# Optimization experiments

Hardware: AMD Instinct MI355X
Metric: run time of the kernel (lower is better)

Reference implementation:

```python
import jax, jax.numpy as jnp
import numpy as np

EPS = 1e-14
RHO = 8.0


def _normalize(x):
    return x / jnp.linalg.norm(x, axis=-1, keepdims=True)


def setup_inputs() -> dict:
    key = jax.random.key(0)
    ks = jax.random.split(key, 12)
    B, D = 4096, 1024
    f = lambda k: _normalize(jax.random.normal(k, (B, D), dtype=jnp.float32))
    pos = lambda k: jax.random.uniform(k, (B, 1), dtype=jnp.float32, minval=0.1, maxval=1.0)
    return {
        "im_feat": f(ks[0]),
        "tt_feat": f(ks[1]),
        "rim_feat": f(ks[2]),
        "rtt_feat": f(ks[3]),
        "remote_u_im": pos(ks[4]),
        "remote_u_tt": pos(ks[5]),
        "loss1_im": pos(ks[6]),
        "loss1_tt": pos(ks[7]),
        "u_im": pos(ks[8]),
        "u_tt": pos(ks[9]),
        "logit_scale": 10.0 * jnp.ones((1,), dtype=jnp.float32),
        "offset": 0,
    }


def _pairwise_loss(rim, rtt, im, tt, logit_scale, offset):
    # features1 = remote, features2 = local (as in forward(): pairwise_loss(remote_features, features, ...))
    sim_image = rim @ tt.T                                  # [B1, B2]
    sim_text = rtt @ im.T                                   # [B1, B2]
    diag_sim = jnp.sum(rim * rtt, axis=-1, keepdims=True)   # [B1, 1]
    exp_im = jnp.exp((sim_image - diag_sim) * logit_scale)
    exp_tt = jnp.exp((sim_text - diag_sim) * logit_scale)
    B1, B2 = sim_image.shape
    # mask zeros the shifted diagonal: equivalent to subtracting the diagonal entry from the row sum
    cols = (jnp.arange(B1) + offset)[:, None]               # [B1, 1]
    rw_sum = B2 - 1 if B1 <= B2 else B2 * (B1 - 1) / B1
    loss_im = (jnp.sum(exp_im, axis=-1, keepdims=True)
               - jnp.take_along_axis(exp_im, cols, axis=1)) / rw_sum
    loss_tt = (jnp.sum(exp_tt, axis=-1, keepdims=True)
               - jnp.take_along_axis(exp_tt, cols, axis=1)) / rw_sum
    return loss_im, loss_tt


def reference(im_feat, tt_feat, rim_feat, rtt_feat, remote_u_im, remote_u_tt,
              loss1_im, loss1_tt, u_im, u_tt, logit_scale, offset):
    loss2_im, loss2_tt = _pairwise_loss(rim_feat, rtt_feat, im_feat, tt_feat, logit_scale, offset)
    pg1 = loss1_im / (u_im + EPS) + loss1_tt / (u_tt + EPS)
    pg2 = loss2_im / (remote_u_im + EPS) + loss2_tt / (remote_u_tt + EPS)
    loss = (jnp.mean(pg1) + jnp.mean(pg2)) / 2
    # multiply_tau branch
    ls = logit_scale[0]
    loss = loss / jax.lax.stop_gradient(ls)
    loss = loss + RHO / ls
    loss = loss + jnp.mean(jnp.log(u_im) + jnp.log(u_tt)) / 2 / ls
    return loss
```

## Files before the change

### kernel.cpp

```cpp
#include <hip/hip_runtime.h>
#include <hip/hip_bf16.h>

#define EPSF 1e-14f
#define RHOF 8.0f

typedef __attribute__((ext_vector_type(4))) float f32x4;
typedef __attribute__((ext_vector_type(8))) int   i32x8;
typedef __attribute__((ext_vector_type(2))) unsigned long long u64x2;

#define AS_GLOBAL __attribute__((address_space(1)))
#define AS_LDS    __attribute__((address_space(3)))


__global__ __launch_bounds__(256) void prep_fp8(
    const float* __restrict__ im,  const float* __restrict__ tt,
    const float* __restrict__ rim, const float* __restrict__ rtt,
    unsigned char* __restrict__ bIm,  unsigned char* __restrict__ bTt,
    unsigned char* __restrict__ bRim, unsigned char* __restrict__ bRtt,
    float* __restrict__ S_im, float* __restrict__ S_tt,
    float* __restrict__ diag, float* __restrict__ red,
    int D, int spm )
{
    __shared__ unsigned char L[8 * 1024];
    const int b = blockIdx.x;
    const int tid = threadIdx.x;
    const int nConv = 4 * spm;
    if (b < nConv) {
        int mIdx = b / spm;
        int slab = b - mIdx * spm;
        const float* src = (mIdx == 0) ? rim : (mIdx == 1) ? tt
                          : (mIdx == 2) ? rtt : im;
        unsigned char* dst = (mIdx == 0) ? bRim : (mIdx == 1) ? bTt
                            : (mIdx == 2) ? bRtt : bIm;
        const float* srow = src + (size_t)slab * 8 * D;
        const int n4 = (8 * D) >> 2;
        for (int idx = tid; idx < n4; idx += 256) {
            float4 v = *(const float4*)(srow + idx * 4);
            int pk = __builtin_amdgcn_cvt_pk_fp8_f32(v.x, v.y, 0, false);
            pk     = __builtin_amdgcn_cvt_pk_fp8_f32(v.z, v.w, pk, true);
            *(int*)&L[idx * 4] = pk;
        }
        __syncthreads();
        const int kTiles = D >> 7;
        const int rb = (slab * 8) >> 7;
        const int r0loc = (slab * 8) & 127;
        for (int g = tid; g < (D >> 1); g += 256) {
            int kb  = g >> 6;
            int rem = g & 63;
            int rl  = rem >> 3;
            int p   = rem & 7;
            int r   = slab * 8 + rl;
            int c   = p ^ (r & 7);
            const unsigned char* lb = &L[rl * D + kb * 128 + c * 16];
            u64x2 o = *(const u64x2*)lb;
            char* outp = (char*)dst
                       + ((size_t)(rb * kTiles + kb) * 1024
                          + (size_t)(r0loc + rl) * 8 + p) * 16;
            *(u64x2*)outp = o;
        }
    } else {
        int db = b - nConv;
        if (db == 0 && tid < 8) red[tid] = 0.f;
        if (tid < 4) { S_im[db * 4 + tid] = 0.f; S_tt[db * 4 + tid] = 0.f; }
        int row  = db * 4 + (tid >> 6);
        int lane = tid & 63;
        const float* a = rim + (size_t)row * D;
        const float* c = rtt + (size_t)row * D;
        float s = 0.f;
        for (int k = lane * 4; k < D; k += 256) {
            float4 av = *(const float4*)(a + k);
            float4 cv = *(const float4*)(c + k);
            s += av.x * cv.x + av.y * cv.y + av.z * cv.z + av.w * cv.w;
        }
        #pragma unroll
        for (int m2 = 1; m2 < 64; m2 <<= 1) s += __shfl_xor(s, m2, 64);
        if (lane == 0) diag[row] = s;
    }
}

__global__ __launch_bounds__(512, 2) void gemm_expsum(
    const unsigned char* __restrict__ A0, const unsigned char* __restrict__ B0,
    float* __restrict__ S0,
    const unsigned char* __restrict__ A1, const unsigned char* __restrict__ B1,
    float* __restrict__ S1,
    const float* __restrict__ logit_scale, const int* __restrict__ offset,
    int Bn, int D)
{
    const int z = blockIdx.z;
    const unsigned char* A = z ? A1 : A0;
    const unsigned char* B = z ? B1 : B0;
    float* S = z ? S1 : S0;

    __shared__ unsigned char As[2][32768];
    __shared__ unsigned char Bs[2][32768];

    const int tid  = threadIdx.x;
    const int wave = tid >> 6;
    const int lane = tid & 63;
    const int lo   = lane & 15;
    const int qd   = lane >> 4;
    const int wm   = wave >> 2;
    const int wn   = wave & 3;
    const int offA = ((2 * qd) ^ (lo & 7)) * 16;

    const int nx  = gridDim.x;
    const int nwg = nx * gridDim.y;
    int wg = blockIdx.y * nx + blockIdx.x;
    int swz = ((nwg & 7) == 0) ? ((wg & 7) * (nwg >> 3) + (wg >> 3)) : wg;
    const int by = swz / nx;
    const int bx = swz - by * nx;

    const int kTiles = D >> 7;
    const unsigned char* Atile = A + (size_t)(2 * by) * kTiles * 16384;
    const unsigned char* Btile = B + (size_t)(2 * bx) * kTiles * 16384;

    const int half = wave >> 1;
    const int part = wave & 1;
    const unsigned char* ownerG =
        (half < 2) ? Atile + (size_t)half * kTiles * 16384
                   : Btile + (size_t)(half - 2) * kTiles * 16384;
    const unsigned char* ownerGL = ownerG + part * 8192 + lane * 16;
    const int ownerLoff = (half & 1) * 16384 + part * 8192;
    const bool ownerIsA = (half < 2);

    auto stageOwner = [&](int buf, int kb) {
        const unsigned char* g = ownerGL + (size_t)kb * 16384;
        unsigned char* l = (ownerIsA ? &As[buf][0] : &Bs[buf][0]) + ownerLoff;
        #pragma unroll
        for (int q = 0; q < 8; ++q)
            __builtin_amdgcn_global_load_lds(
                (const AS_GLOBAL unsigned int*)(g + q * 1024),
                (AS_LDS unsigned int*)(l + q * 1024), 16, 0, 0);
    };

    f32x4 acc[8][4];
    #pragma unroll
    for (int i = 0; i < 8; ++i)
        #pragma unroll
        for (int j = 0; j < 4; ++j)
            acc[i][j] = (f32x4){0.f, 0.f, 0.f, 0.f};

    const int aOff0 = wm * 16384 + lo * 128 + offA;
    const int bOff0 = (wn >> 1) * 16384 + ((wn & 1) * 64 + lo) * 128 + offA;

    stageOwner(0, 0);
    asm volatile("s_waitcnt vmcnt(0)" ::: "memory");
    __builtin_amdgcn_s_barrier();

    for (int kb = 0; kb < kTiles; ++kb) {
        const int cur = kb & 1;
        if (kb + 1 < kTiles)
            stageOwner(1 - cur, kb + 1);

        i32x8 bq[4];
        #pragma unroll
        for (int tj = 0; tj < 4; ++tj) {
            const int ba = bOff0 + tj * 2048;
            union { int4 h[2]; i32x8 v; } u;
            u.h[0] = *(const int4*)&Bs[cur][ba];
            u.h[1] = *(const int4*)&Bs[cur][ba ^ 16];
            bq[tj] = u.v;
        }

        #pragma unroll
        for (int ph = 0; ph < 4; ++ph) {
            const int ti0 = 2 * ph;
            union { int4 h[2]; i32x8 v; } ua0, ua1;
            {
                const int aa0 = aOff0 + ti0 * 2048;
                ua0.h[0] = *(const int4*)&As[cur][aa0];
                ua0.h[1] = *(const int4*)&As[cur][aa0 ^ 16];
                const int aa1 = aOff0 + (ti0 + 1) * 2048;
                ua1.h[0] = *(const int4*)&As[cur][aa1];
                ua1.h[1] = *(const int4*)&As[cur][aa1 ^ 16];
            }
            __builtin_amdgcn_s_barrier();
            __builtin_amdgcn_s_setprio(1);
            #pragma unroll
            for (int tj = 0; tj < 4; ++tj)
                acc[ti0][tj] = __builtin_amdgcn_mfma_scale_f32_16x16x128_f8f6f4(
                    ua0.v, bq[tj], acc[ti0][tj],
                    0, 0, 0, 127, 0, 127);
            #pragma unroll
            for (int tj = 0; tj < 4; ++tj)
                acc[ti0 + 1][tj] = __builtin_amdgcn_mfma_scale_f32_16x16x128_f8f6f4(
                    ua1.v, bq[tj], acc[ti0 + 1][tj],
                    0, 0, 0, 127, 0, 127);
            __builtin_amdgcn_s_setprio(0);
            __builtin_amdgcn_s_barrier();
        }

        if (kb + 1 < kTiles) {
            asm volatile("s_waitcnt vmcnt(0)" ::: "memory");
            __builtin_amdgcn_s_barrier();
        }
    }

    const float ls = logit_scale[0];
    const int offs = offset[0];
    const int rowBase = by * 256 + wm * 128;
    const int colBase = bx * 256 + wn * 64;
    #pragma unroll
    for (int ti = 0; ti < 8; ++ti) {
        #pragma unroll
        for (int r = 0; r < 4; ++r) {
            int gi = rowBase + 16 * ti + 4 * qd + r;
            float rs = 0.f;
            #pragma unroll
            for (int tj = 0; tj < 4; ++tj) {
                int gj = colBase + 16 * tj + lo;
                float e = __expf(ls * acc[ti][tj][r]);
                if (gj == gi + offs) e = 0.f;
                rs += e;
            }
            #pragma unroll
            for (int m = 1; m < 16; m <<= 1) rs += __shfl_xor(rs, m, 64);
            if (lo == 0) atomicAdd(&S[gi], rs);
        }
    }
}

__global__ __launch_bounds__(256) void final_kernel(
    const float* __restrict__ S_im, const float* __restrict__ S_tt,
    const float* __restrict__ diag,
    const float* __restrict__ ru_im, const float* __restrict__ ru_tt,
    const float* __restrict__ l1_im, const float* __restrict__ l1_tt,
    const float* __restrict__ u_im,  const float* __restrict__ u_tt,
    const float* __restrict__ logit_scale, float* __restrict__ red,
    float* __restrict__ out, int Bn)
{
    const float ls = logit_scale[0];
    const float inv_rw = 1.0f / (float)(Bn - 1);
    const int gid = blockIdx.x * 256 + threadIdx.x;
    float pg = 0.f, lg = 0.f;
    for (int i = gid; i < Bn; i += 8 * 256) {
        float p1 = l1_im[i] / (u_im[i] + EPSF) + l1_tt[i] / (u_tt[i] + EPSF);
        float dd = expf(-ls * diag[i]);
        float p2 = dd * S_im[i] * inv_rw / (ru_im[i] + EPSF)
                 + dd * S_tt[i] * inv_rw / (ru_tt[i] + EPSF);
        pg += p1 + p2;
        lg += logf(u_im[i]) + logf(u_tt[i]);
    }
    __shared__ float sp[256], sl[256];
    sp[threadIdx.x] = pg; sl[threadIdx.x] = lg;
    __syncthreads();
    for (int s = 128; s > 0; s >>= 1) {
        if (threadIdx.x < s) { sp[threadIdx.x] += sp[threadIdx.x + s];
                               sl[threadIdx.x] += sl[threadIdx.x + s]; }
        __syncthreads();
    }
    if (threadIdx.x == 0) {
        atomicAdd(&red[0], sp[0]);
        atomicAdd(&red[1], sl[0]);
        __threadfence();
        int t = atomicAdd((int*)&red[2], 1);
        if (t == gridDim.x - 1) {
            float pgSum = atomicAdd(&red[0], 0.f);
            float lgSum = atomicAdd(&red[1], 0.f);
            float loss = ((pgSum / (float)Bn) * 0.5f) / ls
                       + RHOF / ls
                       + (lgSum / (float)Bn) * 0.5f / ls;
            out[0] = loss;
        }
    }
}

extern "C" void kernel_launch(void* const* d_in, const int* in_sizes, int n_in,
                              void* d_out, int out_size, void* d_ws, size_t ws_size,
                              hipStream_t stream) {
    const float* im    = (const float*)d_in[0];
    const float* tt    = (const float*)d_in[1];
    const float* rim   = (const float*)d_in[2];
    const float* rtt   = (const float*)d_in[3];
    const float* ru_im = (const float*)d_in[4];
    const float* ru_tt = (const float*)d_in[5];
    const float* l1_im = (const float*)d_in[6];
    const float* l1_tt = (const float*)d_in[7];
    const float* u_im  = (const float*)d_in[8];
    const float* u_tt  = (const float*)d_in[9];
    const float* lsc   = (const float*)d_in[10];
    const int*   offs  = (const int*)d_in[11];

    const int Bn = in_sizes[4];
    const int D  = in_sizes[0] / Bn;
    const int spm = Bn / 8;

    char* base = (char*)d_ws;
    float* S_im = (float*)base;
    float* S_tt = S_im + Bn;
    float* diag = S_tt + Bn;
    float* red  = diag + Bn;
    const size_t headBytes = (((size_t)(3 * Bn + 8) * sizeof(float)) + 255) & ~(size_t)255;
    const size_t matBytes  = (size_t)Bn * D;
    unsigned char* buf0 = (unsigned char*)(base + headBytes);
    unsigned char* bRim = buf0;
    unsigned char* bTt  = buf0 + matBytes;
    unsigned char* bRtt = buf0 + 2 * matBytes;
    unsigned char* bIm  = buf0 + 3 * matBytes;

    prep_fp8<<<4 * spm + Bn / 4, 256, 0, stream>>>(
        im, tt, rim, rtt, bIm, bTt, bRim, bRtt, S_im, S_tt, diag, red, D, spm);

    dim3 ggrid(Bn / 256, Bn / 256, 2);
    gemm_expsum<<<ggrid, 512, 0, stream>>>(bRim, bTt, S_im, bRtt, bIm, S_tt,
                                           lsc, offs, Bn, D);

    final_kernel<<<8, 256, 0, stream>>>(S_im, S_tt, diag, ru_im, ru_tt,
                                        l1_im, l1_tt, u_im, u_tt, lsc,
                                        red, (float*)d_out, Bn);
}
```

Baseline: 178.0 us.

## Fuse both GEMMs into one persistent block loop and simplify fp8 prep

The GEMM kernel now runs both similarity products (rim·tt and rtt·im) inside each block instead of using a z-dimension of 2. It prefetches the first k-tile of the second product during the last tile of the first, which hides the pipeline prologue and the epilogue. Grid size halves, so each block does twice the work, and occupancy on 256 CUs drops from 512 to 256 blocks. The fp8 conversion kernel drops its LDS staging and writes swizzled 16-byte chunks directly per thread. The final reduction also gets more blocks.

```diff
diff --git a/kernel.cpp b/kernel.cpp
--- a/kernel.cpp
+++ b/kernel.cpp
@@ -6,7 +6,6 @@
 
 typedef __attribute__((ext_vector_type(4))) float f32x4;
 typedef __attribute__((ext_vector_type(8))) int   i32x8;
-typedef __attribute__((ext_vector_type(2))) unsigned long long u64x2;
 
 #define AS_GLOBAL __attribute__((address_space(1)))
 #define AS_LDS    __attribute__((address_space(3)))
@@ -19,45 +18,42 @@
     unsigned char* __restrict__ bRim, unsigned char* __restrict__ bRtt,
     float* __restrict__ S_im, float* __restrict__ S_tt,
     float* __restrict__ diag, float* __restrict__ red,
-    int D, int spm )
+    int D, int bpm )
 {
-    __shared__ unsigned char L[8 * 1024];
     const int b = blockIdx.x;
     const int tid = threadIdx.x;
-    const int nConv = 4 * spm;
+    const int nConv = 4 * bpm;
     if (b < nConv) {
-        int mIdx = b / spm;
-        int slab = b - mIdx * spm;
+        int mIdx = b / bpm;
+        int blk  = b - mIdx * bpm;
         const float* src = (mIdx == 0) ? rim : (mIdx == 1) ? tt
                           : (mIdx == 2) ? rtt : im;
         unsigned char* dst = (mIdx == 0) ? bRim : (mIdx == 1) ? bTt
                             : (mIdx == 2) ? bRtt : bIm;
-        const float* srow = src + (size_t)slab * 8 * D;
-        const int n4 = (8 * D) >> 2;
-        for (int idx = tid; idx < n4; idx += 256) {
-            float4 v = *(const float4*)(srow + idx * 4);
-            int pk = __builtin_amdgcn_cvt_pk_fp8_f32(v.x, v.y, 0, false);
-            pk     = __builtin_amdgcn_cvt_pk_fp8_f32(v.z, v.w, pk, true);
-            *(int*)&L[idx * 4] = pk;
-        }
-        __syncthreads();
+        const int upr = D >> 4;
+        const int rpb = 256 / upr;
+        const int urow = tid / upr;
+        const int c    = tid - urow * upr;
+        const int r    = blk * rpb + urow;
         const int kTiles = D >> 7;
-        const int rb = (slab * 8) >> 7;
-        const int r0loc = (slab * 8) & 127;
-        for (int g = tid; g < (D >> 1); g += 256) {
-            int kb  = g >> 6;
-            int rem = g & 63;
-            int rl  = rem >> 3;
-            int p   = rem & 7;
-            int r   = slab * 8 + rl;
-            int c   = p ^ (r & 7);
-            const unsigned char* lb = &L[rl * D + kb * 128 + c * 16];
-            u64x2 o = *(const u64x2*)lb;
-            char* outp = (char*)dst
-                       + ((size_t)(rb * kTiles + kb) * 1024
-                          + (size_t)(r0loc + rl) * 8 + p) * 16;
-            *(u64x2*)outp = o;
-        }
+        const float* p = src + (size_t)r * D + (size_t)c * 16;
+        float4 v0 = ((const float4*)p)[0];
+        float4 v1 = ((const float4*)p)[1];
+        float4 v2 = ((const float4*)p)[2];
+        float4 v3 = ((const float4*)p)[3];
+        int w0 = __builtin_amdgcn_cvt_pk_fp8_f32(v0.x, v0.y, 0, false);
+        w0     = __builtin_amdgcn_cvt_pk_fp8_f32(v0.z, v0.w, w0, true);
+        int w1 = __builtin_amdgcn_cvt_pk_fp8_f32(v1.x, v1.y, 0, false);
+        w1     = __builtin_amdgcn_cvt_pk_fp8_f32(v1.z, v1.w, w1, true);
+        int w2 = __builtin_amdgcn_cvt_pk_fp8_f32(v2.x, v2.y, 0, false);
+        w2     = __builtin_amdgcn_cvt_pk_fp8_f32(v2.z, v2.w, w2, true);
+        int w3 = __builtin_amdgcn_cvt_pk_fp8_f32(v3.x, v3.y, 0, false);
+        w3     = __builtin_amdgcn_cvt_pk_fp8_f32(v3.z, v3.w, w3, true);
+        int4 out = make_int4(w0, w1, w2, w3);
+        const int kb = c >> 3;
+        const int p8 = (c & 7) ^ (r & 7);
+        *(int4*)(dst + ((size_t)((r >> 7) * kTiles + kb) * 1024
+                        + (size_t)(r & 127) * 8 + p8) * 16) = out;
     } else {
         int db = b - nConv;
         if (db == 0 && tid < 8) red[tid] = 0.f;
@@ -65,11 +61,11 @@
         int row  = db * 4 + (tid >> 6);
         int lane = tid & 63;
         const float* a = rim + (size_t)row * D;
-        const float* c = rtt + (size_t)row * D;
+        const float* c2 = rtt + (size_t)row * D;
         float s = 0.f;
         for (int k = lane * 4; k < D; k += 256) {
             float4 av = *(const float4*)(a + k);
-            float4 cv = *(const float4*)(c + k);
+            float4 cv = *(const float4*)(c2 + k);
             s += av.x * cv.x + av.y * cv.y + av.z * cv.z + av.w * cv.w;
         }
         #pragma unroll
@@ -86,11 +82,6 @@
     const float* __restrict__ logit_scale, const int* __restrict__ offset,
     int Bn, int D)
 {
-    const int z = blockIdx.z;
-    const unsigned char* A = z ? A1 : A0;
-    const unsigned char* B = z ? B1 : B0;
-    float* S = z ? S1 : S0;
-
     __shared__ unsigned char As[2][32768];
     __shared__ unsigned char Bs[2][32768];
 
@@ -111,20 +102,18 @@
     const int bx = swz - by * nx;
 
     const int kTiles = D >> 7;
-    const unsigned char* Atile = A + (size_t)(2 * by) * kTiles * 16384;
-    const unsigned char* Btile = B + (size_t)(2 * bx) * kTiles * 16384;
 
     const int half = wave >> 1;
     const int part = wave & 1;
-    const unsigned char* ownerG =
-        (half < 2) ? Atile + (size_t)half * kTiles * 16384
-                   : Btile + (size_t)(half - 2) * kTiles * 16384;
-    const unsigned char* ownerGL = ownerG + part * 8192 + lane * 16;
+    const bool ownerIsA = (half < 2);
     const int ownerLoff = (half & 1) * 16384 + part * 8192;
-    const bool ownerIsA = (half < 2);
-
-    auto stageOwner = [&](int buf, int kb) {
-        const unsigned char* g = ownerGL + (size_t)kb * 16384;
+
+    auto stageOwner = [&](int buf, const unsigned char* At,
+                          const unsigned char* Bt, int kb) {
+        const unsigned char* g =
+            (ownerIsA ? At + (size_t)half * kTiles * 16384
+                      : Bt + (size_t)(half - 2) * kTiles * 16384)
+            + (size_t)kb * 16384 + part * 8192 + lane * 16;
         unsigned char* l = (ownerIsA ? &As[buf][0] : &Bs[buf][0]) + ownerLoff;
         #pragma unroll
         for (int q = 0; q < 8; ++q)
@@ -133,89 +122,110 @@
                 (AS_LDS unsigned int*)(l + q * 1024), 16, 0, 0);
     };
 
-    f32x4 acc[8][4];
-    #pragma unroll
-    for (int i = 0; i < 8; ++i)
-        #pragma unroll
-        for (int j = 0; j < 4; ++j)
-            acc[i][j] = (f32x4){0.f, 0.f, 0.f, 0.f};
-
     const int aOff0 = wm * 16384 + lo * 128 + offA;
     const int bOff0 = (wn >> 1) * 16384 + ((wn & 1) * 64 + lo) * 128 + offA;
 
-    stageOwner(0, 0);
-    asm volatile("s_waitcnt vmcnt(0)" ::: "memory");
-    __builtin_amdgcn_s_barrier();
-
-    for (int kb = 0; kb < kTiles; ++kb) {
-        const int cur = kb & 1;
-        if (kb + 1 < kTiles)
-            stageOwner(1 - cur, kb + 1);
-
-        i32x8 bq[4];
+    const float ls = logit_scale[0];
+    const int offs = offset[0];
+
+    for (int zz = 0; zz < 2; ++zz) {
+        const unsigned char* A = zz ? A1 : A0;
+        const unsigned char* B = zz ? B1 : B0;
+        float* S = zz ? S1 : S0;
+        const unsigned char* Atile = A + (size_t)(2 * by) * kTiles * 16384;
+        const unsigned char* Btile = B + (size_t)(2 * bx) * kTiles * 16384;
+
+        f32x4 acc[8][4];
         #pragma unroll
-        for (int tj = 0; tj < 4; ++tj) {
-            const int ba = bOff0 + tj * 2048;
-            union { int4 h[2]; i32x8 v; } u;
-            u.h[0] = *(const int4*)&Bs[cur][ba];
-            u.h[1] = *(const int4*)&Bs[cur][ba ^ 16];
-            bq[tj] = u.v;
-        }
-
-        #pragma unroll
-        for (int ph = 0; ph < 4; ++ph) {
-            const int ti0 = 2 * ph;
-            union { int4 h[2]; i32x8 v; } ua0, ua1;
-            {
-                const int aa0 = aOff0 + ti0 * 2048;
-                ua0.h[0] = *(const int4*)&As[cur][aa0];
-                ua0.h[1] = *(const int4*)&As[cur][aa0 ^ 16];
-                const int aa1 = aOff0 + (ti0 + 1) * 2048;
-                ua1.h[0] = *(const int4*)&As[cur][aa1];
-                ua1.h[1] = *(const int4*)&As[cur][aa1 ^ 16];
-            }
-            __builtin_amdgcn_s_barrier();
-            __builtin_amdgcn_s_setprio(1);
+        for (int i = 0; i < 8; ++i)
             #pragma unroll
-            for (int tj = 0; tj < 4; ++tj)
-                acc[ti0][tj] = __builtin_amdgcn_mfma_scale_f32_16x16x128_f8f6f4(
-                    ua0.v, bq[tj], acc[ti0][tj],
-                    0, 0, 0, 127, 0, 127);
-            #pragma unroll
-            for (int tj = 0; tj < 4; ++tj)
-                acc[ti0 + 1][tj] = __builtin_amdgcn_mfma_scale_f32_16x16x128_f8f6f4(
-                    ua1.v, bq[tj], acc[ti0 + 1][tj],
-                    0, 0, 0, 127, 0, 127);
-            __builtin_amdgcn_s_setprio(0);
-            __builtin_amdgcn_s_barrier();
-        }
-
-        if (kb + 1 < kTiles) {
+            for (int j = 0; j < 4; ++j)
+                acc[i][j] = (f32x4){0.f, 0.f, 0.f, 0.f};
+
+        if (zz == 0) {
+            stageOwner(0, Atile, Btile, 0);
             asm volatile("s_waitcnt vmcnt(0)" ::: "memory");
             __builtin_amdgcn_s_barrier();
         }
-    }
-
-    const float ls = logit_scale[0];
-    const int offs = offset[0];
-    const int rowBase = by * 256 + wm * 128;
-    const int colBase = bx * 256 + wn * 64;
-    #pragma unroll
-    for (int ti = 0; ti < 8; ++ti) {
-        #pragma unroll
-        for (int r = 0; r < 4; ++r) {
-            int gi = rowBase + 16 * ti + 4 * qd + r;
-            float rs = 0.f;
+
+        for (int kb = 0; kb < kTiles; ++kb) {
+            const int cur = kb & 1;
+            if (kb + 1 < kTiles) {
+                stageOwner(1 - cur, Atile, Btile, kb + 1);
+            } else if (zz == 0) {
+                stageOwner(1 - cur,
+                           A1 + (size_t)(2 * by) * kTiles * 16384,
+                           B1 + (size_t)(2 * bx) * kTiles * 16384, 0);
+            }
+
+            i32x8 bq[4];
             #pragma unroll
             for (int tj = 0; tj < 4; ++tj) {
-                int gj = colBase + 16 * tj + lo;
-                float e = __expf(ls * acc[ti][tj][r]);
-                if (gj == gi + offs) e = 0.f;
-                rs += e;
-            }
+                const int ba = bOff0 + tj * 2048;
+                union { int4 h[2]; i32x8 v; } u;
+                u.h[0] = *(const int4*)&Bs[cur][ba];
+                u.h[1] = *(const int4*)&Bs[cur][ba ^ 16];
+                bq[tj] = u.v;
+            }
+
             #pragma unroll
-            for (int m = 1; m < 16; m <<= 1) rs += __shfl_xor(rs, m, 64);
-            if (lo == 0) atomicAdd(&S[gi], rs);
+            for (int ph = 0; ph < 4; ++ph) {
+                const int ti0 = 2 * ph;
+                union { int4 h[2]; i32x8 v; } ua0, ua1;
+                {
+                    const int aa0 = aOff0 + ti0 * 2048;
+                    ua0.h[0] = *(const int4*)&As[cur][aa0];
+                    ua0.h[1] = *(const int4*)&As[cur][aa0 ^ 16];
+                    const int aa1 = aOff0 + (ti0 + 1) * 2048;
+                    ua1.h[0] = *(const int4*)&As[cur][aa1];
+                    ua1.h[1] = *(const int4*)&As[cur][aa1 ^ 16];
+                }
+                __builtin_amdgcn_s_barrier();
+                __builtin_amdgcn_s_setprio(1);
+                #pragma unroll
+                for (int tj = 0; tj < 4; ++tj)
+                    acc[ti0][tj] = __builtin_amdgcn_mfma_scale_f32_16x16x128_f8f6f4(
+                        ua0.v, bq[tj], acc[ti0][tj],
+                        0, 0, 0, 127, 0, 127);
+                #pragma unroll
+                for (int tj = 0; tj < 4; ++tj)
+                    acc[ti0 + 1][tj] = __builtin_amdgcn_mfma_scale_f32_16x16x128_f8f6f4(
+                        ua1.v, bq[tj], acc[ti0 + 1][tj],
+                        0, 0, 0, 127, 0, 127);
+                __builtin_amdgcn_s_setprio(0);
+                __builtin_amdgcn_s_barrier();
+            }
+
+            if (kb + 1 < kTiles) {
+                asm volatile("s_waitcnt vmcnt(0)" ::: "memory");
+                __builtin_amdgcn_s_barrier();
+            }
+        }
+
+        const int rowBase = by * 256 + wm * 128;
+        const int colBase = bx * 256 + wn * 64;
+        #pragma unroll
+        for (int ti = 0; ti < 8; ++ti) {
+            #pragma unroll
+            for (int r = 0; r < 4; ++r) {
+                int gi = rowBase + 16 * ti + 4 * qd + r;
+                float rs = 0.f;
+                #pragma unroll
+                for (int tj = 0; tj < 4; ++tj) {
+                    int gj = colBase + 16 * tj + lo;
+                    float e = __expf(ls * acc[ti][tj][r]);
+                    if (gj == gi + offs) e = 0.f;
+                    rs += e;
+                }
+                #pragma unroll
+                for (int m = 1; m < 16; m <<= 1) rs += __shfl_xor(rs, m, 64);
+                if (lo == 0) atomicAdd(&S[gi], rs);
+            }
+        }
+
+        if (zz == 0) {
+            asm volatile("s_waitcnt vmcnt(0)" ::: "memory");
+            __builtin_amdgcn_s_barrier();
         }
     }
 }
@@ -232,8 +242,9 @@
     const float ls = logit_scale[0];
     const float inv_rw = 1.0f / (float)(Bn - 1);
     const int gid = blockIdx.x * 256 + threadIdx.x;
+    const int stride = gridDim.x * 256;
     float pg = 0.f, lg = 0.f;
-    for (int i = gid; i < Bn; i += 8 * 256) {
+    for (int i = gid; i < Bn; i += stride) {
         float p1 = l1_im[i] / (u_im[i] + EPSF) + l1_tt[i] / (u_tt[i] + EPSF);
         float dd = expf(-ls * diag[i]);
         float p2 = dd * S_im[i] * inv_rw / (ru_im[i] + EPSF)
@@ -283,7 +294,8 @@
 
     const int Bn = in_sizes[4];
     const int D  = in_sizes[0] / Bn;
-    const int spm = Bn / 8;
+    const int rpb = 4096 / D;
+    const int bpm = Bn / rpb;
 
     char* base = (char*)d_ws;
     float* S_im = (float*)base;
@@ -298,14 +310,14 @@
     unsigned char* bRtt = buf0 + 2 * matBytes;
     unsigned char* bIm  = buf0 + 3 * matBytes;
 
-    prep_fp8<<<4 * spm + Bn / 4, 256, 0, stream>>>(
-        im, tt, rim, rtt, bIm, bTt, bRim, bRtt, S_im, S_tt, diag, red, D, spm);
-
-    dim3 ggrid(Bn / 256, Bn / 256, 2);
+    prep_fp8<<<4 * bpm + Bn / 4, 256, 0, stream>>>(
+        im, tt, rim, rtt, bIm, bTt, bRim, bRtt, S_im, S_tt, diag, red, D, bpm);
+
+    dim3 ggrid(Bn / 256, Bn / 256, 1);
     gemm_expsum<<<ggrid, 512, 0, stream>>>(bRim, bTt, S_im, bRtt, bIm, S_tt,
                                            lsc, offs, Bn, D);
 
-    final_kernel<<<8, 256, 0, stream>>>(S_im, S_tt, diag, ru_im, ru_tt,
-                                        l1_im, l1_tt, u_im, u_tt, lsc,
-                                        red, (float*)d_out, Bn);
+    final_kernel<<<32, 256, 0, stream>>>(S_im, S_tt, diag, ru_im, ru_tt,
+                                         l1_im, l1_tt, u_im, u_tt, lsc,
+                                         red, (float*)d_out, Bn);
 }
```

Measured after the change: 176.9 us. No clear change (-0.6%).
